# Kernel optimization log

Measured on AMD Instinct MI355X. Metric: run time of the kernel, lower is better.

Reference implementation:

```python
import jax, jax.numpy as jnp
import numpy as np

D_MODEL = 1024
NUM_HEADS = 16
DIM_HEAD = 64
B, NQ, NKV = 2, 2048, 2048


def setup_inputs() -> dict:
    key = jax.random.key(0)
    ks = jax.random.split(key, 12)
    inner = NUM_HEADS * DIM_HEAD
    s_in = 1.0 / np.sqrt(D_MODEL)
    s_o = 1.0 / np.sqrt(inner)
    return {
        "Q": jax.random.normal(ks[0], (B, NQ, D_MODEL), jnp.float32),
        "K": jax.random.normal(ks[1], (B, NKV, D_MODEL), jnp.float32),
        "V": jax.random.normal(ks[2], (B, NKV, D_MODEL), jnp.float32),
        "mask": jax.random.randint(ks[3], (B, 1, NQ, NKV), 0, 2, jnp.int32),
        "W_q": jax.random.normal(ks[4], (D_MODEL, inner), jnp.float32) * s_in,
        "b_q": jnp.zeros((inner,), jnp.float32),
        "W_k": jax.random.normal(ks[5], (D_MODEL, inner), jnp.float32) * s_in,
        "b_k": jnp.zeros((inner,), jnp.float32),
        "W_v": jax.random.normal(ks[6], (D_MODEL, inner), jnp.float32) * s_in,
        "b_v": jnp.zeros((inner,), jnp.float32),
        "W_o": jax.random.normal(ks[7], (inner, D_MODEL), jnp.float32) * s_o,
        "b_o": jnp.zeros((D_MODEL,), jnp.float32),
    }


def reference(Q, K, V, mask, W_q, b_q, W_k, b_k, W_v, b_v, W_o, b_o):
    h, d = NUM_HEADS, DIM_HEAD
    # projections: [b, n, h*d] -> [b, h, n, d]
    def split_heads(x):
        b, n, _ = x.shape
        return x.reshape(b, n, h, d).transpose(0, 2, 1, 3)

    q = split_heads(Q @ W_q + b_q)
    k = split_heads(K @ W_k + b_k)
    v = split_heads(V @ W_v + b_v)

    scores = jnp.einsum("bhqd,bhkd->bhqk", q, k) / jnp.sqrt(jnp.float32(d))
    scores = jnp.where(mask == 0, jnp.float32(-1e9), scores)
    probs = jax.nn.softmax(scores, axis=-1)
    out = jnp.einsum("bhqk,bhkd->bhqd", probs, v)
    out = out.transpose(0, 2, 1, 3).reshape(Q.shape[0], Q.shape[1], h * d)
    return out @ W_o + b_o
```

## Files before the change

### kernel.cpp

```cpp
#include <hip/hip_runtime.h>
#include <hip/hip_bf16.h>
#include <stdint.h>

#define DM   1024
#define NH   16
#define DHD  64
#define BB   2
#define NQS  2048
#define NKVS 2048

typedef __attribute__((ext_vector_type(8))) short short8;
typedef __attribute__((ext_vector_type(4))) float f32x4;
typedef __attribute__((ext_vector_type(4))) unsigned short us4;

static __device__ __forceinline__ unsigned short f2bf(float f) {
  union { float f; unsigned u; } v; v.f = f;
  unsigned r = (v.u + 0x7fffu + ((v.u >> 16) & 1u)) >> 16;
  return (unsigned short)r;
}

#define MFMA(a, b, c) __builtin_amdgcn_mfma_f32_16x16x32_bf16((a), (b), (c), 0, 0, 0)

__global__ __launch_bounds__(256) void wt_kernel(
    const float* __restrict__ Wq, const float* __restrict__ Wk,
    const float* __restrict__ Wv, const float* __restrict__ Wo,
    unsigned short* __restrict__ wt) {
  __shared__ unsigned short Ls[64][68];
  const int z = blockIdx.z;
  const float* W = (z == 0) ? Wq : (z == 1) ? Wk : (z == 2) ? Wv : Wo;
  unsigned short* out = wt + (size_t)z * 1024 * 1024;
  const int r0 = blockIdx.y * 64, c0 = blockIdx.x * 64;
  const int t = threadIdx.x;
#pragma unroll
  for (int i = 0; i < 4; i++) {
    int idx = t + 256 * i;
    int row = idx >> 4, c4 = (idx & 15) * 4;
    float4 v = *(const float4*)(W + (size_t)(r0 + row) * 1024 + c0 + c4);
    Ls[row][c4 + 0] = f2bf(v.x);
    Ls[row][c4 + 1] = f2bf(v.y);
    Ls[row][c4 + 2] = f2bf(v.z);
    Ls[row][c4 + 3] = f2bf(v.w);
  }
  __syncthreads();
#pragma unroll
  for (int i = 0; i < 4; i++) {
    int idx = t + 256 * i;
    int jj = idx >> 4, k4 = (idx & 15) * 4;
    us4 o;
    o[0] = Ls[k4 + 0][jj];
    o[1] = Ls[k4 + 1][jj];
    o[2] = Ls[k4 + 2][jj];
    o[3] = Ls[k4 + 3][jj];
    *(us4*)(out + (size_t)(c0 + jj) * 1024 + r0 + k4) = o;
  }
}

__global__ __launch_bounds__(256) void maskpack_kernel(
    const int* __restrict__ mask, unsigned long long* __restrict__ pk) {
  const long long total = (long long)BB * NQS * NKVS;
  const long long stride = (long long)gridDim.x * 256;
  for (long long i = (long long)blockIdx.x * 256 + threadIdx.x; i < total; i += stride) {
    int m = mask[i];
    unsigned long long b = __ballot(m != 0);
    if ((i & 63) == 0) pk[i >> 6] = b;
  }
}

__global__ __launch_bounds__(256) void proj_kernel(
    const float* __restrict__ Qin, const float* __restrict__ Kin, const float* __restrict__ Vin,
    const unsigned short* __restrict__ wt,
    const float* __restrict__ bq, const float* __restrict__ bk, const float* __restrict__ bv,
    unsigned short* __restrict__ q_ws, unsigned short* __restrict__ k_ws,
    unsigned short* __restrict__ v_ws) {
  __shared__ unsigned short As[128 * 72];
  __shared__ unsigned short Bs[128 * 72];
  const int z = blockIdx.z;
  const float* X = (z == 0) ? Qin : (z == 1) ? Kin : Vin;
  const float* bias = (z == 0) ? bq : (z == 1) ? bk : bv;
  const unsigned short* Wt = wt + (size_t)z * 1024 * 1024;
  const int m0 = blockIdx.y * 128, j0 = blockIdx.x * 128;
  const int t = threadIdx.x, wid = t >> 6, lane = t & 63, lr = lane & 15, lg = lane >> 4;
  const int wm = wid >> 1, wn = wid & 1;

  f32x4 acc[4][4] = {};
  for (int kt = 0; kt < 16; kt++) {
    const int k0 = kt * 64;
#pragma unroll
    for (int i = 0; i < 8; i++) {
      int idx = t + 256 * i;
      int row = idx >> 4, c4 = (idx & 15) * 4;
      float4 v = *(const float4*)(X + (size_t)(m0 + row) * 1024 + k0 + c4);
      us4 o;
      o[0] = f2bf(v.x); o[1] = f2bf(v.y); o[2] = f2bf(v.z); o[3] = f2bf(v.w);
      *(us4*)(&As[row * 72 + c4]) = o;
    }
#pragma unroll
    for (int i = 0; i < 4; i++) {
      int idx = t + 256 * i;
      int j = idx >> 3, c8 = (idx & 7) * 8;
      short8 v = *(const short8*)(Wt + (size_t)(j0 + j) * 1024 + k0 + c8);
      *(short8*)(&Bs[j * 72 + c8]) = v;
    }
    __syncthreads();
    short8 a[2][4], b[2][4];
#pragma unroll
    for (int ks = 0; ks < 2; ks++)
#pragma unroll
      for (int mf = 0; mf < 4; mf++)
        a[ks][mf] = *(const short8*)(&As[(wm * 64 + mf * 16 + lr) * 72 + ks * 32 + lg * 8]);
#pragma unroll
    for (int ks = 0; ks < 2; ks++)
#pragma unroll
      for (int nf = 0; nf < 4; nf++)
        b[ks][nf] = *(const short8*)(&Bs[(wn * 64 + nf * 16 + lr) * 72 + ks * 32 + lg * 8]);
#pragma unroll
    for (int ks = 0; ks < 2; ks++)
#pragma unroll
      for (int mf = 0; mf < 4; mf++)
#pragma unroll
        for (int nf = 0; nf < 4; nf++)
          acc[mf][nf] = MFMA(a[ks][mf], b[ks][nf], acc[mf][nf]);
    __syncthreads();
  }
#pragma unroll
  for (int nf = 0; nf < 4; nf++) {
    const int j = j0 + wn * 64 + nf * 16 + lr;
    const float bj = bias[j];
    const int h = j >> 6, dd = j & 63;
#pragma unroll
    for (int mf = 0; mf < 4; mf++) {
      const int mb = m0 + wm * 64 + mf * 16 + lg * 4;
      const int b_ = mb >> 11, nb = mb & 2047;
      if (z == 2) {
        us4 o;
#pragma unroll
        for (int r = 0; r < 4; r++) o[r] = f2bf(acc[mf][nf][r] + bj);
        *(us4*)(v_ws + ((size_t)(b_ * NH + h) * DHD + dd) * NKVS + nb) = o;
      } else {
        unsigned short* dst = (z == 0) ? q_ws : k_ws;
        const float sc = (z == 0) ? 0.125f : 1.0f;
#pragma unroll
        for (int r = 0; r < 4; r++) {
          float val = (acc[mf][nf][r] + bj) * sc;
          dst[((size_t)(b_ * NH + h) * NQS + nb + r) * DHD + dd] = f2bf(val);
        }
      }
    }
  }
}

__global__ __launch_bounds__(256) void attn_kernel(
    const unsigned short* __restrict__ q_ws, const unsigned short* __restrict__ k_ws,
    const unsigned short* __restrict__ v_ws, const unsigned long long* __restrict__ pk,
    unsigned short* __restrict__ o_ws) {
  __shared__ unsigned char Pl[4][2048];
  const int qt = blockIdx.x, h = blockIdx.y, b = blockIdx.z;
  const int bh = b * NH + h;
  const int t = threadIdx.x, wid = t >> 6, lane = t & 63, lr = lane & 15, lg = lane >> 4;
  const int q = qt * 64 + wid * 16 + lr;

  const size_t qoff = ((size_t)bh * NQS + q) * DHD + lg * 8;
  const short8 qb0 = *(const short8*)(q_ws + qoff);
  const short8 qb1 = *(const short8*)(q_ws + qoff + 32);

  const unsigned long long* mp = pk + ((size_t)b * NQS + q) * 32;
  const unsigned short* kbase = k_ws + (size_t)bh * NQS * DHD;
  const unsigned short* vbase = v_ws + (size_t)bh * DHD * NKVS;

  unsigned char* Pb = &Pl[wid][0];
  const unsigned wsw = (unsigned)(lr * 128) ^ ((unsigned)(lr & 7) << 4);

  f32x4 O[4] = {};
  float m = -1e30f, l = 0.f;

  for (int kt = 0; kt < 32; kt++) {
    const int kv0 = kt * 64;
    f32x4 s[4];
    __builtin_amdgcn_s_setprio(1);
#pragma unroll
    for (int cf = 0; cf < 4; cf++) {
      const unsigned short* kp = kbase + (size_t)(kv0 + cf * 16 + lr) * DHD + lg * 8;
      short8 ka0 = *(const short8*)(kp);
      short8 ka1 = *(const short8*)(kp + 32);
      f32x4 zz = {};
      s[cf] = MFMA(ka0, qb0, zz);
      s[cf] = MFMA(ka1, qb1, s[cf]);
    }
    __builtin_amdgcn_s_setprio(0);
    const unsigned long long mw = mp[kt];
    float pmax = -1e30f;
#pragma unroll
    for (int cf = 0; cf < 4; cf++)
#pragma unroll
      for (int r = 0; r < 4; r++) {
        const bool bit = (mw >> (cf * 16 + lg * 4 + r)) & 1ull;
        const float v = bit ? s[cf][r] : -1e30f;
        s[cf][r] = v;
        pmax = fmaxf(pmax, v);
      }
    pmax = fmaxf(pmax, __shfl_xor(pmax, 16));
    pmax = fmaxf(pmax, __shfl_xor(pmax, 32));
    if (!__all(pmax - m <= 8.f)) {
      const float mn = fmaxf(m, pmax);
      const float sc = __expf(m - mn);
      m = mn;
      l *= sc;
#pragma unroll
      for (int df = 0; df < 4; df++)
#pragma unroll
        for (int r = 0; r < 4; r++) O[df][r] *= sc;
    }
    float rs = 0.f;
#pragma unroll
    for (int cf = 0; cf < 4; cf++) {
      unsigned pu0, pu1;
      {
        const float p0 = (s[cf][0] > -1e29f) ? __expf(s[cf][0] - m) : 0.f;
        const float p1 = (s[cf][1] > -1e29f) ? __expf(s[cf][1] - m) : 0.f;
        rs += p0 + p1;
        pu0 = (unsigned)f2bf(p0) | ((unsigned)f2bf(p1) << 16);
      }
      {
        const float p0 = (s[cf][2] > -1e29f) ? __expf(s[cf][2] - m) : 0.f;
        const float p1 = (s[cf][3] > -1e29f) ? __expf(s[cf][3] - m) : 0.f;
        rs += p0 + p1;
        pu1 = (unsigned)f2bf(p0) | ((unsigned)f2bf(p1) << 16);
      }
      *(uint2*)(Pb + (wsw ^ (unsigned)(cf * 32 + lg * 8))) = make_uint2(pu0, pu1);
    }
    rs += __shfl_xor(rs, 16);
    rs += __shfl_xor(rs, 32);
    l += rs;
    const short8 pb0 = *(const short8*)(Pb + (wsw ^ (unsigned)(lg * 16)));
    const short8 pb1 = *(const short8*)(Pb + (wsw ^ (unsigned)(64 + lg * 16)));
    __builtin_amdgcn_s_setprio(1);
#pragma unroll
    for (int df = 0; df < 4; df++) {
      const unsigned short* vp = vbase + (size_t)(df * 16 + lr) * NKVS + kv0 + lg * 8;
      short8 va0 = *(const short8*)(vp);
      short8 va1 = *(const short8*)(vp + 32);
      O[df] = MFMA(va0, pb0, O[df]);
      O[df] = MFMA(va1, pb1, O[df]);
    }
    __builtin_amdgcn_s_setprio(0);
  }
  const float rinv = (l > 0.f) ? 1.f / l : 0.f;
#pragma unroll
  for (int df = 0; df < 4; df++) {
    us4 o;
#pragma unroll
    for (int r = 0; r < 4; r++) o[r] = f2bf(O[df][r] * rinv);
    *(us4*)(o_ws + ((size_t)b * NQS + q) * DM + h * DHD + df * 16 + lg * 4) = o;
  }
}

__global__ __launch_bounds__(256) void outproj_kernel(
    const unsigned short* __restrict__ Ain, const unsigned short* __restrict__ Wt,
    const float* __restrict__ bo, float* __restrict__ out) {
  __shared__ unsigned short As[128 * 72];
  __shared__ unsigned short Bs[128 * 72];
  const int m0 = blockIdx.y * 128, j0 = blockIdx.x * 128;
  const int t = threadIdx.x, wid = t >> 6, lane = t & 63, lr = lane & 15, lg = lane >> 4;
  const int wm = wid >> 1, wn = wid & 1;

  f32x4 acc[4][4] = {};
  for (int kt = 0; kt < 16; kt++) {
    const int k0 = kt * 64;
#pragma unroll
    for (int i = 0; i < 4; i++) {
      int idx = t + 256 * i;
      int row = idx >> 3, c8 = (idx & 7) * 8;
      *(short8*)(&As[row * 72 + c8]) =
          *(const short8*)(Ain + (size_t)(m0 + row) * 1024 + k0 + c8);
    }
#pragma unroll
    for (int i = 0; i < 4; i++) {
      int idx = t + 256 * i;
      int j = idx >> 3, c8 = (idx & 7) * 8;
      *(short8*)(&Bs[j * 72 + c8]) =
          *(const short8*)(Wt + (size_t)(j0 + j) * 1024 + k0 + c8);
    }
    __syncthreads();
    short8 a[2][4], b[2][4];
#pragma unroll
    for (int ks = 0; ks < 2; ks++)
#pragma unroll
      for (int mf = 0; mf < 4; mf++)
        a[ks][mf] = *(const short8*)(&As[(wm * 64 + mf * 16 + lr) * 72 + ks * 32 + lg * 8]);
#pragma unroll
    for (int ks = 0; ks < 2; ks++)
#pragma unroll
      for (int nf = 0; nf < 4; nf++)
        b[ks][nf] = *(const short8*)(&Bs[(wn * 64 + nf * 16 + lr) * 72 + ks * 32 + lg * 8]);
#pragma unroll
    for (int ks = 0; ks < 2; ks++)
#pragma unroll
      for (int mf = 0; mf < 4; mf++)
#pragma unroll
        for (int nf = 0; nf < 4; nf++)
          acc[mf][nf] = MFMA(a[ks][mf], b[ks][nf], acc[mf][nf]);
    __syncthreads();
  }
#pragma unroll
  for (int nf = 0; nf < 4; nf++) {
    const int j = j0 + wn * 64 + nf * 16 + lr;
    const float bj = bo[j];
#pragma unroll
    for (int mf = 0; mf < 4; mf++) {
      const int mb = m0 + wm * 64 + mf * 16 + lg * 4;
#pragma unroll
      for (int r = 0; r < 4; r++)
        out[(size_t)(mb + r) * 1024 + j] = acc[mf][nf][r] + bj;
    }
  }
}

extern "C" void kernel_launch(void* const* d_in, const int* in_sizes, int n_in,
                              void* d_out, int out_size, void* d_ws, size_t ws_size,
                              hipStream_t stream) {
  (void)in_sizes; (void)n_in; (void)out_size; (void)ws_size;
  const float* Q  = (const float*)d_in[0];
  const float* K  = (const float*)d_in[1];
  const float* V  = (const float*)d_in[2];
  const int* mask = (const int*)d_in[3];
  const float* Wq = (const float*)d_in[4];
  const float* bq = (const float*)d_in[5];
  const float* Wk = (const float*)d_in[6];
  const float* bk = (const float*)d_in[7];
  const float* Wv = (const float*)d_in[8];
  const float* bv = (const float*)d_in[9];
  const float* Wo = (const float*)d_in[10];
  const float* bo = (const float*)d_in[11];
  float* out = (float*)d_out;

  char* ws = (char*)d_ws;
  const size_t SZ_BHND = (size_t)BB * NH * NQS * DHD * 2;
  unsigned short* q_ws = (unsigned short*)(ws);
  unsigned short* k_ws = (unsigned short*)(ws + SZ_BHND);
  unsigned short* v_ws = (unsigned short*)(ws + 2 * SZ_BHND);
  unsigned short* o_ws = (unsigned short*)(ws + 3 * SZ_BHND);
  unsigned short* wt   = (unsigned short*)(ws + 4 * SZ_BHND);
  unsigned long long* pk = (unsigned long long*)(ws + 5 * SZ_BHND);

  hipLaunchKernelGGL(wt_kernel, dim3(16, 16, 4), dim3(256), 0, stream, Wq, Wk, Wv, Wo, wt);
  hipLaunchKernelGGL(maskpack_kernel, dim3(4096), dim3(256), 0, stream, mask, pk);
  hipLaunchKernelGGL(proj_kernel, dim3(8, 32, 3), dim3(256), 0, stream,
                     Q, K, V, wt, bq, bk, bv, q_ws, k_ws, v_ws);
  hipLaunchKernelGGL(attn_kernel, dim3(32, 16, 2), dim3(256), 0, stream,
                     q_ws, k_ws, v_ws, pk, o_ws);
  hipLaunchKernelGGL(outproj_kernel, dim3(8, 32), dim3(256), 0, stream,
                     o_ws, wt + (size_t)3 * 1024 * 1024, bo, out);
}
```

Baseline: 479.2 us.

## Rewrite attention with 32x32 MFMA, register P exchange, and split-KV across waves

The attention kernel now uses 32x32x16 bf16 MFMA tiles, with each wave handling 32 queries and half of the KV range. Two waves per query tile process the two KV halves and merge their softmax states through shared memory at the end. The P matrix is rearranged with lane shuffles instead of an LDS round-trip. This is meant to raise MFMA efficiency and remove LDS traffic, at the cost of more registers per thread, a final combine with a block barrier, and a smaller query tile per wave.

```diff
diff --git a/kernel.cpp b/kernel.cpp
--- a/kernel.cpp
+++ b/kernel.cpp
@@ -11,6 +11,7 @@
 
 typedef __attribute__((ext_vector_type(8))) short short8;
 typedef __attribute__((ext_vector_type(4))) float f32x4;
+typedef __attribute__((ext_vector_type(16))) float f32x16;
 typedef __attribute__((ext_vector_type(4))) unsigned short us4;
 
 static __device__ __forceinline__ unsigned short f2bf(float f) {
@@ -19,7 +20,8 @@
   return (unsigned short)r;
 }
 
-#define MFMA(a, b, c) __builtin_amdgcn_mfma_f32_16x16x32_bf16((a), (b), (c), 0, 0, 0)
+#define MFMA(a, b, c)   __builtin_amdgcn_mfma_f32_16x16x32_bf16((a), (b), (c), 0, 0, 0)
+#define MFMA32(a, b, c) __builtin_amdgcn_mfma_f32_32x32x16_bf16((a), (b), (c), 0, 0, 0)
 
 __global__ __launch_bounds__(256) void wt_kernel(
     const float* __restrict__ Wq, const float* __restrict__ Wk,
@@ -153,104 +155,128 @@
     const unsigned short* __restrict__ q_ws, const unsigned short* __restrict__ k_ws,
     const unsigned short* __restrict__ v_ws, const unsigned long long* __restrict__ pk,
     unsigned short* __restrict__ o_ws) {
-  __shared__ unsigned char Pl[4][2048];
-  const int qt = blockIdx.x, h = blockIdx.y, b = blockIdx.z;
+  __shared__ float Ml[2][64][2];
+  __shared__ float Ol[2][64][36];
+  const int h = blockIdx.y, b = blockIdx.z;
   const int bh = b * NH + h;
-  const int t = threadIdx.x, wid = t >> 6, lane = t & 63, lr = lane & 15, lg = lane >> 4;
-  const int q = qt * 64 + wid * 16 + lr;
-
-  const size_t qoff = ((size_t)bh * NQS + q) * DHD + lg * 8;
-  const short8 qb0 = *(const short8*)(q_ws + qoff);
-  const short8 qb1 = *(const short8*)(q_ws + qoff + 32);
-
+  const int t = threadIdx.x, wid = t >> 6, lane = t & 63;
+  const int l31 = lane & 31, hi = lane >> 5;
+  const int qsub = wid & 1, kvh = wid >> 1;
+  const int q = blockIdx.x * 64 + qsub * 32 + l31;
+
+  short8 qb[4];
+  {
+    const unsigned short* qp = q_ws + ((size_t)bh * NQS + q) * DHD + hi * 8;
+#pragma unroll
+    for (int ks = 0; ks < 4; ks++) qb[ks] = *(const short8*)(qp + ks * 16);
+  }
   const unsigned long long* mp = pk + ((size_t)b * NQS + q) * 32;
   const unsigned short* kbase = k_ws + (size_t)bh * NQS * DHD;
   const unsigned short* vbase = v_ws + (size_t)bh * DHD * NKVS;
 
-  unsigned char* Pb = &Pl[wid][0];
-  const unsigned wsw = (unsigned)(lr * 128) ^ ((unsigned)(lr & 7) << 4);
-
-  f32x4 O[4] = {};
+  f32x16 O[2] = {};
   float m = -1e30f, l = 0.f;
 
-  for (int kt = 0; kt < 32; kt++) {
-    const int kv0 = kt * 64;
-    f32x4 s[4];
-    __builtin_amdgcn_s_setprio(1);
-#pragma unroll
-    for (int cf = 0; cf < 4; cf++) {
-      const unsigned short* kp = kbase + (size_t)(kv0 + cf * 16 + lr) * DHD + lg * 8;
-      short8 ka0 = *(const short8*)(kp);
-      short8 ka1 = *(const short8*)(kp + 32);
-      f32x4 zz = {};
-      s[cf] = MFMA(ka0, qb0, zz);
-      s[cf] = MFMA(ka1, qb1, s[cf]);
-    }
-    __builtin_amdgcn_s_setprio(0);
-    const unsigned long long mw = mp[kt];
-    float pmax = -1e30f;
-#pragma unroll
-    for (int cf = 0; cf < 4; cf++)
-#pragma unroll
-      for (int r = 0; r < 4; r++) {
-        const bool bit = (mw >> (cf * 16 + lg * 4 + r)) & 1ull;
-        const float v = bit ? s[cf][r] : -1e30f;
-        s[cf][r] = v;
-        pmax = fmaxf(pmax, v);
-      }
-    pmax = fmaxf(pmax, __shfl_xor(pmax, 16));
-    pmax = fmaxf(pmax, __shfl_xor(pmax, 32));
-    if (!__all(pmax - m <= 8.f)) {
-      const float mn = fmaxf(m, pmax);
-      const float sc = __expf(m - mn);
-      m = mn;
-      l *= sc;
-#pragma unroll
-      for (int df = 0; df < 4; df++)
-#pragma unroll
-        for (int r = 0; r < 4; r++) O[df][r] *= sc;
-    }
-    float rs = 0.f;
-#pragma unroll
-    for (int cf = 0; cf < 4; cf++) {
-      unsigned pu0, pu1;
+  for (int it = 0; it < 16; it++) {
+    const unsigned long long mw = mp[kvh * 16 + it];
+#pragma unroll
+    for (int st = 0; st < 2; st++) {
+      const int kv0 = kvh * 1024 + it * 64 + st * 32;
+      const unsigned mword = st ? (unsigned)(mw >> 32) : (unsigned)mw;
+      f32x16 S = {};
       {
-        const float p0 = (s[cf][0] > -1e29f) ? __expf(s[cf][0] - m) : 0.f;
-        const float p1 = (s[cf][1] > -1e29f) ? __expf(s[cf][1] - m) : 0.f;
-        rs += p0 + p1;
-        pu0 = (unsigned)f2bf(p0) | ((unsigned)f2bf(p1) << 16);
-      }
-      {
-        const float p0 = (s[cf][2] > -1e29f) ? __expf(s[cf][2] - m) : 0.f;
-        const float p1 = (s[cf][3] > -1e29f) ? __expf(s[cf][3] - m) : 0.f;
-        rs += p0 + p1;
-        pu1 = (unsigned)f2bf(p0) | ((unsigned)f2bf(p1) << 16);
-      }
-      *(uint2*)(Pb + (wsw ^ (unsigned)(cf * 32 + lg * 8))) = make_uint2(pu0, pu1);
-    }
-    rs += __shfl_xor(rs, 16);
-    rs += __shfl_xor(rs, 32);
-    l += rs;
-    const short8 pb0 = *(const short8*)(Pb + (wsw ^ (unsigned)(lg * 16)));
-    const short8 pb1 = *(const short8*)(Pb + (wsw ^ (unsigned)(64 + lg * 16)));
-    __builtin_amdgcn_s_setprio(1);
-#pragma unroll
-    for (int df = 0; df < 4; df++) {
-      const unsigned short* vp = vbase + (size_t)(df * 16 + lr) * NKVS + kv0 + lg * 8;
-      short8 va0 = *(const short8*)(vp);
-      short8 va1 = *(const short8*)(vp + 32);
-      O[df] = MFMA(va0, pb0, O[df]);
-      O[df] = MFMA(va1, pb1, O[df]);
-    }
-    __builtin_amdgcn_s_setprio(0);
-  }
-  const float rinv = (l > 0.f) ? 1.f / l : 0.f;
-#pragma unroll
-  for (int df = 0; df < 4; df++) {
-    us4 o;
-#pragma unroll
-    for (int r = 0; r < 4; r++) o[r] = f2bf(O[df][r] * rinv);
-    *(us4*)(o_ws + ((size_t)b * NQS + q) * DM + h * DHD + df * 16 + lg * 4) = o;
+        const unsigned short* kp = kbase + (size_t)(kv0 + l31) * DHD + hi * 8;
+#pragma unroll
+        for (int ks = 0; ks < 4; ks++)
+          S = MFMA32(*(const short8*)(kp + ks * 16), qb[ks], S);
+      }
+      float p[16];
+      float pmax = -1e30f;
+#pragma unroll
+      for (int r = 0; r < 16; r++) {
+        const int kvr = (r & 3) + 8 * (r >> 2) + 4 * hi;
+        const bool bit = (mword >> kvr) & 1u;
+        const float sv = bit ? S[r] : -1e30f;
+        p[r] = sv;
+        pmax = fmaxf(pmax, sv);
+      }
+      pmax = fmaxf(pmax, __shfl_xor(pmax, 32));
+      if (!__all(pmax - m <= 8.f)) {
+        const float mn = fmaxf(m, pmax);
+        const float sc = __expf(m - mn);
+        m = mn; l *= sc;
+#pragma unroll
+        for (int dt = 0; dt < 2; dt++)
+#pragma unroll
+          for (int r = 0; r < 16; r++) O[dt][r] *= sc;
+      }
+      float rs = 0.f;
+#pragma unroll
+      for (int r = 0; r < 16; r++) {
+        p[r] = (p[r] > -1e29f) ? __expf(p[r] - m) : 0.f;
+        rs += p[r];
+      }
+      rs += __shfl_xor(rs, 32);
+      l += rs;
+      unsigned pk8[8], sw[8];
+#pragma unroll
+      for (int i = 0; i < 8; i++)
+        pk8[i] = (unsigned)f2bf(p[2 * i]) | ((unsigned)f2bf(p[2 * i + 1]) << 16);
+#pragma unroll
+      for (int i = 0; i < 8; i++) sw[i] = __shfl_xor(pk8[i], 32);
+      union { unsigned u[4]; short8 s; } pb0, pb1;
+      pb0.u[0] = hi ? sw[2] : pk8[0];
+      pb0.u[1] = hi ? sw[3] : pk8[1];
+      pb0.u[2] = hi ? pk8[2] : sw[0];
+      pb0.u[3] = hi ? pk8[3] : sw[1];
+      pb1.u[0] = hi ? sw[6] : pk8[4];
+      pb1.u[1] = hi ? sw[7] : pk8[5];
+      pb1.u[2] = hi ? pk8[6] : sw[4];
+      pb1.u[3] = hi ? pk8[7] : sw[5];
+#pragma unroll
+      for (int dt = 0; dt < 2; dt++) {
+        const unsigned short* vp = vbase + (size_t)(dt * 32 + l31) * NKVS + kv0 + hi * 8;
+        short8 va0 = *(const short8*)(vp);
+        short8 va1 = *(const short8*)(vp + 16);
+        O[dt] = MFMA32(va0, pb0.s, O[dt]);
+        O[dt] = MFMA32(va1, pb1.s, O[dt]);
+      }
+    }
+  }
+  if (kvh == 1) {
+    Ml[qsub][lane][0] = m;
+    Ml[qsub][lane][1] = l;
+#pragma unroll
+    for (int dt = 0; dt < 2; dt++)
+#pragma unroll
+      for (int g = 0; g < 4; g++) {
+        f32x4 v;
+#pragma unroll
+        for (int j = 0; j < 4; j++) v[j] = O[dt][g * 4 + j];
+        *(f32x4*)&Ol[qsub][lane][dt * 16 + g * 4] = v;
+      }
+  }
+  __syncthreads();
+  if (kvh == 0) {
+    const float m1 = Ml[qsub][lane][0], l1 = Ml[qsub][lane][1];
+    const float M = fmaxf(m, m1);
+    const float a0 = __expf(m - M), a1 = __expf(m1 - M);
+    const float L = l * a0 + l1 * a1;
+    const float rinv = (L > 0.f) ? 1.f / L : 0.f;
+    const float s0 = a0 * rinv, s1 = a1 * rinv;
+#pragma unroll
+    for (int dt = 0; dt < 2; dt++)
+#pragma unroll
+      for (int g = 0; g < 4; g++) {
+        us4 o;
+#pragma unroll
+        for (int j = 0; j < 4; j++) {
+          const float v = O[dt][g * 4 + j] * s0 + Ol[qsub][lane][dt * 16 + g * 4 + j] * s1;
+          o[j] = f2bf(v);
+        }
+        const int d = dt * 32 + g * 8 + hi * 4;
+        *(us4*)(o_ws + ((size_t)b * NQS + q) * DM + h * DHD + d) = o;
+      }
   }
 }
 
```

Result: faster. 399.7 us (-16.6%).
